# Kernel optimization log

Measured on AMD Instinct MI355X. Metric: run time of the kernel, lower is better.

Reference implementation:

```python
import jax, jax.numpy as jnp
import numpy as np


def setup_inputs() -> dict:
    key = jax.random.key(0)
    k1, k2, k3 = jax.random.split(key, 3)
    B, H, S, D = 4, 16, 2048, 64
    queries = jax.random.normal(k1, (B, H, S, D), dtype=jnp.float32)
    keys = jax.random.normal(k2, (B, H, S, D), dtype=jnp.float32)
    values = jax.random.normal(k3, (B, H, S, D), dtype=jnp.float32)
    return {"queries": queries, "keys": keys, "values": values, "d_k": D}


def reference(queries, keys, values, d_k):
    # scores = Q K^T / sqrt(d_k)  -> [B, H, S, S]
    scale = 1.0 / jnp.sqrt(jnp.asarray(d_k, dtype=queries.dtype))
    scores = jnp.einsum("bhqd,bhkd->bhqk", queries, keys) * scale
    weights = jax.nn.softmax(scores, axis=-1)
    # out = weights V -> [B, H, S, D]
    return jnp.einsum("bhqk,bhkd->bhqd", weights, values)
```

## Files before the change

kernel.cpp:

```cpp
#include <hip/hip_runtime.h>
#include <hip/hip_bf16.h>

typedef __attribute__((ext_vector_type(8))) short short8;
typedef __attribute__((ext_vector_type(4))) short short4v;
typedef __attribute__((ext_vector_type(16))) float f32x16;

constexpr int Sn = 2048, Dn = 64;
constexpr int KVB = 64;
constexpr int QB  = 256;
constexpr int NT  = Sn / KVB;
constexpr int KSTR = 72;
constexpr int VSTR = 68;
constexpr float QSC = 0.18033688011112042f;

struct SMemS { short K[2][KVB][KSTR]; short Vt[2][Dn][VSTR]; };
union  SMem  { SMemS s; float ep[4][32][36]; };

__device__ inline unsigned cvt_pk_bf16(float a, float b) {
  unsigned r;
  asm("v_cvt_pk_bf16_f32 %0, %1, %2" : "=v"(r) : "v"(a), "v"(b));
  return r;
}
__device__ inline short8 catw(unsigned a, unsigned b, unsigned c, unsigned d) {
  union { unsigned u[4]; short8 s; } t;
  t.u[0]=a; t.u[1]=b; t.u[2]=c; t.u[3]=d;
  return t.s;
}
__device__ inline short8 pack8(float4 a, float4 b) {
  return catw(cvt_pk_bf16(a.x,a.y), cvt_pk_bf16(a.z,a.w),
              cvt_pk_bf16(b.x,b.y), cvt_pk_bf16(b.z,b.w));
}
__device__ inline short8 cat4(short4v a, short4v b) {
  short8 r;
  r[0]=a[0]; r[1]=a[1]; r[2]=a[2]; r[3]=a[3];
  r[4]=b[0]; r[5]=b[1]; r[6]=b[2]; r[7]=b[3];
  return r;
}

__global__ __launch_bounds__(256, 2)
void attn_fwd(const float* __restrict__ Qm, const float* __restrict__ Km,
              const float* __restrict__ Vm, float* __restrict__ Om) {
  __shared__ alignas(16) SMem sm;

  const int fid = blockIdx.x + (blockIdx.y << 3);
  const int xcd = fid & 7, w = fid >> 3;
  const int qt = w & 7, bh = (xcd << 3) | (w >> 3);

  const size_t base = (size_t)bh * Sn * Dn;
  const float* Qb = Qm + base;
  const float* Kb = Km + base;
  const float* Vb = Vm + base;
  float*       Ob = Om + base;

  const int tid = threadIdx.x, wv = tid >> 6, lane = tid & 63;
  const int il = lane & 31, hi = lane >> 5;
  const int qr0 = qt * QB + wv * 64;

  short8 qf[2][4];
#pragma unroll
  for (int u = 0; u < 2; ++u)
#pragma unroll
    for (int ks = 0; ks < 4; ++ks) {
      const float4* qp = (const float4*)(Qb + (size_t)(qr0 + u*32 + il) * Dn + ks*16 + hi*8);
      float4 a = qp[0], b = qp[1];
      a.x*=QSC; a.y*=QSC; a.z*=QSC; a.w*=QSC;
      b.x*=QSC; b.y*=QSC; b.z*=QSC; b.w*=QSC;
      qf[u][ks] = pack8(a, b);
    }

  f32x16 acc[2][2];
#pragma unroll
  for (int u = 0; u < 2; ++u)
#pragma unroll
    for (int dt = 0; dt < 2; ++dt)
#pragma unroll
      for (int r = 0; r < 16; ++r) acc[u][dt][r] = 0.f;
  float m_run[2] = {-1e30f, -1e30f}, l_run[2] = {0.f, 0.f};

  f32x16 fz;
#pragma unroll
  for (int r = 0; r < 16; ++r) fz[r] = 0.f;

  const int krow = tid >> 2, kc = (tid & 3) * 16;
  const int vd = tid & 63, vk0 = (tid >> 6) * 8;

  auto stageK = [&](int buf, float4 a0, float4 a1, float4 a2, float4 a3) {
    *(short8*)&sm.s.K[buf][krow][kc]     = pack8(a0, a1);
    *(short8*)&sm.s.K[buf][krow][kc + 8] = pack8(a2, a3);
  };
  auto stageV = [&](int buf, const float* vv) {
#pragma unroll
    for (int c = 0; c < 2; ++c) {
      union { unsigned u[2]; short4v s; } t0, t1;
      t0.u[0] = cvt_pk_bf16(vv[c*8+0], vv[c*8+1]);
      t0.u[1] = cvt_pk_bf16(vv[c*8+2], vv[c*8+3]);
      t1.u[0] = cvt_pk_bf16(vv[c*8+4], vv[c*8+5]);
      t1.u[1] = cvt_pk_bf16(vv[c*8+6], vv[c*8+7]);
      short* p = &sm.s.Vt[buf][vd][vk0 + c*32];
      *(short4v*)p       = t0.s;
      *(short4v*)(p + 4) = t1.s;
    }
  };

  short8 pb[2][2][2];

  auto qk_sm = [&](int buf) {
    short8 kf[2][4];
#pragma unroll
    for (int h = 0; h < 2; ++h)
#pragma unroll
      for (int ks = 0; ks < 4; ++ks)
        kf[h][ks] = *(const short8*)&sm.s.K[buf][h*32 + il][ks*16 + hi*8];

    f32x16 sa[2][2];
#pragma unroll
    for (int u = 0; u < 2; ++u)
#pragma unroll
      for (int h = 0; h < 2; ++h) {
        sa[u][h] = __builtin_amdgcn_mfma_f32_32x32x16_bf16(kf[h][0], qf[u][0], fz, 0, 0, 0);
#pragma unroll
        for (int ks = 1; ks < 4; ++ks)
          sa[u][h] = __builtin_amdgcn_mfma_f32_32x32x16_bf16(kf[h][ks], qf[u][ks], sa[u][h], 0, 0, 0);
      }

#pragma unroll
    for (int u = 0; u < 2; ++u) {
      float tm[16];
#pragma unroll
      for (int r = 0; r < 16; ++r) tm[r] = fmaxf(sa[u][0][r], sa[u][1][r]);
#pragma unroll
      for (int s = 8; s > 0; s >>= 1)
#pragma unroll
        for (int r = 0; r < s; ++r) tm[r] = fmaxf(tm[r], tm[r + s]);
      float mx = fmaxf(tm[0], __shfl_xor(tm[0], 32));

      float mnew = fmaxf(m_run[u], mx);
      float corr = __builtin_amdgcn_exp2f(m_run[u] - mnew);
      m_run[u] = mnew;
      l_run[u] *= corr;
#pragma unroll
      for (int dt = 0; dt < 2; ++dt)
#pragma unroll
        for (int r = 0; r < 16; ++r) acc[u][dt][r] *= corr;

#pragma unroll
      for (int h = 0; h < 2; ++h)
#pragma unroll
        for (int r = 0; r < 16; ++r) sa[u][h][r] = __builtin_amdgcn_exp2f(sa[u][h][r] - mnew);
      float ta[16];
#pragma unroll
      for (int r = 0; r < 16; ++r) ta[r] = sa[u][0][r] + sa[u][1][r];
#pragma unroll
      for (int s = 8; s > 0; s >>= 1)
#pragma unroll
        for (int r = 0; r < s; ++r) ta[r] += ta[r + s];
      l_run[u] += ta[0] + __shfl_xor(ta[0], 32);

#pragma unroll
      for (int h = 0; h < 2; ++h) {
        pb[u][h][0] = catw(cvt_pk_bf16(sa[u][h][0],  sa[u][h][1]),  cvt_pk_bf16(sa[u][h][2],  sa[u][h][3]),
                           cvt_pk_bf16(sa[u][h][4],  sa[u][h][5]),  cvt_pk_bf16(sa[u][h][6],  sa[u][h][7]));
        pb[u][h][1] = catw(cvt_pk_bf16(sa[u][h][8],  sa[u][h][9]),  cvt_pk_bf16(sa[u][h][10], sa[u][h][11]),
                           cvt_pk_bf16(sa[u][h][12], sa[u][h][13]), cvt_pk_bf16(sa[u][h][14], sa[u][h][15]));
      }
    }
  };

  auto pv = [&](int buf) {
#pragma unroll
    for (int h = 0; h < 2; ++h)
#pragma unroll
      for (int dt = 0; dt < 2; ++dt) {
        const short* vrow = &sm.s.Vt[buf][dt*32 + il][h*32];
        short8 va = cat4(*(const short4v*)(vrow + 4*hi),      *(const short4v*)(vrow + 8  + 4*hi));
        short8 vb = cat4(*(const short4v*)(vrow + 16 + 4*hi), *(const short4v*)(vrow + 24 + 4*hi));
#pragma unroll
        for (int u = 0; u < 2; ++u) {
          acc[u][dt] = __builtin_amdgcn_mfma_f32_32x32x16_bf16(va, pb[u][h][0], acc[u][dt], 0, 0, 0);
          acc[u][dt] = __builtin_amdgcn_mfma_f32_32x32x16_bf16(vb, pb[u][h][1], acc[u][dt], 0, 0, 0);
        }
      }
  };

  {
    const float4* kp = (const float4*)(Kb + (size_t)krow * Dn + kc);
    float4 a0 = kp[0], a1 = kp[1], a2 = kp[2], a3 = kp[3];
    float vv[16];
#pragma unroll
    for (int c = 0; c < 2; ++c)
#pragma unroll
      for (int j = 0; j < 8; ++j) vv[c*8+j] = Vb[(size_t)(vk0 + c*32 + j) * Dn + vd];
    stageK(0, a0, a1, a2, a3);
    stageV(0, vv);
  }
  __syncthreads();

  int cur = 0;
#pragma unroll 1
  for (int t = 0; t < NT - 1; ++t) {
    const int kvn = (t + 1) * KVB;
    const float4* kp = (const float4*)(Kb + (size_t)(kvn + krow) * Dn + kc);
    float4 na0 = kp[0], na1 = kp[1], na2 = kp[2], na3 = kp[3];
    float nv[16];
#pragma unroll
    for (int c = 0; c < 2; ++c)
#pragma unroll
      for (int j = 0; j < 8; ++j) nv[c*8+j] = Vb[(size_t)(kvn + vk0 + c*32 + j) * Dn + vd];

    qk_sm(cur);
    stageK(cur ^ 1, na0, na1, na2, na3);
    stageV(cur ^ 1, nv);
    pv(cur);
    __syncthreads();
    cur ^= 1;
  }
  qk_sm(cur);
  pv(cur);
  __syncthreads();

  const int q2 = lane >> 1, dh = (lane & 1) * 16;
#pragma unroll
  for (int u = 0; u < 2; ++u) {
    const float inv = 1.0f / l_run[u];
#pragma unroll
    for (int dt = 0; dt < 2; ++dt) {
#pragma unroll
      for (int r = 0; r < 16; ++r) {
        int dcol = (r & 3) + 8 * (r >> 2) + 4 * hi;
        sm.ep[wv][il][dcol] = acc[u][dt][r] * inv;
      }
#pragma unroll
      for (int i = 0; i < 4; ++i) {
        float4 o = *(const float4*)&sm.ep[wv][q2][dh + i*4];
        *(float4*)(Ob + (size_t)(qr0 + u*32 + q2) * Dn + dt*32 + dh + i*4) = o;
      }
    }
  }
}

extern "C" void kernel_launch(void* const* d_in, const int* in_sizes, int n_in,
                              void* d_out, int out_size, void* d_ws, size_t ws_size,
                              hipStream_t stream) {
  const float* Q = (const float*)d_in[0];
  const float* K = (const float*)d_in[1];
  const float* V = (const float*)d_in[2];
  float* O = (float*)d_out;
  dim3 grid(Sn / QB, 4 * 16);
  attn_fwd<<<grid, 256, 0, stream>>>(Q, K, V, O);
}
```

Baseline: 104.4 us.

## Software-pipeline PV of previous tile with QK of current tile

```diff
diff --git a/kernel.cpp b/kernel.cpp
--- a/kernel.cpp
+++ b/kernel.cpp
@@ -76,6 +76,9 @@
 #pragma unroll
       for (int r = 0; r < 16; ++r) acc[u][dt][r] = 0.f;
   float m_run[2] = {-1e30f, -1e30f}, l_run[2] = {0.f, 0.f};
+  float corrp[2] = {0.f, 0.f};
+  short8 pb[2][2][2];
+  short8 vregs[8];
 
   f32x16 fz;
 #pragma unroll
@@ -84,35 +87,42 @@
   const int krow = tid >> 2, kc = (tid & 3) * 16;
   const int vd = tid & 63, vk0 = (tid >> 6) * 8;
 
-  auto stageK = [&](int buf, float4 a0, float4 a1, float4 a2, float4 a3) {
-    *(short8*)&sm.s.K[buf][krow][kc]     = pack8(a0, a1);
-    *(short8*)&sm.s.K[buf][krow][kc + 8] = pack8(a2, a3);
-  };
-  auto stageV = [&](int buf, const float* vv) {
+  auto loadK = [&](int t, short8& k0, short8& k1) {
+    const float4* kp = (const float4*)(Kb + (size_t)(t*KVB + krow) * Dn + kc);
+    k0 = pack8(kp[0], kp[1]);
+    k1 = pack8(kp[2], kp[3]);
+  };
+  auto loadV = [&](int t, short4v* v4) {
 #pragma unroll
     for (int c = 0; c < 2; ++c) {
+      float vv[8];
+#pragma unroll
+      for (int j = 0; j < 8; ++j) vv[j] = Vb[(size_t)(t*KVB + vk0 + c*32 + j) * Dn + vd];
       union { unsigned u[2]; short4v s; } t0, t1;
-      t0.u[0] = cvt_pk_bf16(vv[c*8+0], vv[c*8+1]);
-      t0.u[1] = cvt_pk_bf16(vv[c*8+2], vv[c*8+3]);
-      t1.u[0] = cvt_pk_bf16(vv[c*8+4], vv[c*8+5]);
-      t1.u[1] = cvt_pk_bf16(vv[c*8+6], vv[c*8+7]);
+      t0.u[0] = cvt_pk_bf16(vv[0], vv[1]); t0.u[1] = cvt_pk_bf16(vv[2], vv[3]);
+      t1.u[0] = cvt_pk_bf16(vv[4], vv[5]); t1.u[1] = cvt_pk_bf16(vv[6], vv[7]);
+      v4[c*2]   = t0.s;
+      v4[c*2+1] = t1.s;
+    }
+  };
+  auto writeKV = [&](int buf, short8 k0, short8 k1, const short4v* v4) {
+    *(short8*)&sm.s.K[buf][krow][kc]     = k0;
+    *(short8*)&sm.s.K[buf][krow][kc + 8] = k1;
+#pragma unroll
+    for (int c = 0; c < 2; ++c) {
       short* p = &sm.s.Vt[buf][vd][vk0 + c*32];
-      *(short4v*)p       = t0.s;
-      *(short4v*)(p + 4) = t1.s;
-    }
-  };
-
-  short8 pb[2][2][2];
-
-  auto qk_sm = [&](int buf) {
+      *(short4v*)p       = v4[c*2];
+      *(short4v*)(p + 4) = v4[c*2+1];
+    }
+  };
+
+  auto qk = [&](int buf, f32x16 sa[2][2]) {
     short8 kf[2][4];
 #pragma unroll
     for (int h = 0; h < 2; ++h)
 #pragma unroll
       for (int ks = 0; ks < 4; ++ks)
         kf[h][ks] = *(const short8*)&sm.s.K[buf][h*32 + il][ks*16 + hi*8];
-
-    f32x16 sa[2][2];
 #pragma unroll
     for (int u = 0; u < 2; ++u)
 #pragma unroll
@@ -122,7 +132,9 @@
         for (int ks = 1; ks < 4; ++ks)
           sa[u][h] = __builtin_amdgcn_mfma_f32_32x32x16_bf16(kf[h][ks], qf[u][ks], sa[u][h], 0, 0, 0);
       }
-
+  };
+
+  auto softmax = [&](f32x16 sa[2][2]) {
 #pragma unroll
     for (int u = 0; u < 2; ++u) {
       float tm[16];
@@ -137,12 +149,8 @@
       float mnew = fmaxf(m_run[u], mx);
       float corr = __builtin_amdgcn_exp2f(m_run[u] - mnew);
       m_run[u] = mnew;
+      corrp[u] = corr;
       l_run[u] *= corr;
-#pragma unroll
-      for (int dt = 0; dt < 2; ++dt)
-#pragma unroll
-        for (int r = 0; r < 16; ++r) acc[u][dt][r] *= corr;
-
 #pragma unroll
       for (int h = 0; h < 2; ++h)
 #pragma unroll
@@ -166,56 +174,77 @@
     }
   };
 
-  auto pv = [&](int buf) {
+  auto vload = [&](int buf) {
 #pragma unroll
     for (int h = 0; h < 2; ++h)
 #pragma unroll
       for (int dt = 0; dt < 2; ++dt) {
         const short* vrow = &sm.s.Vt[buf][dt*32 + il][h*32];
-        short8 va = cat4(*(const short4v*)(vrow + 4*hi),      *(const short4v*)(vrow + 8  + 4*hi));
-        short8 vb = cat4(*(const short4v*)(vrow + 16 + 4*hi), *(const short4v*)(vrow + 24 + 4*hi));
+        vregs[h*4 + dt*2 + 0] = cat4(*(const short4v*)(vrow + 4*hi),      *(const short4v*)(vrow + 8  + 4*hi));
+        vregs[h*4 + dt*2 + 1] = cat4(*(const short4v*)(vrow + 16 + 4*hi), *(const short4v*)(vrow + 24 + 4*hi));
+      }
+  };
+
+  auto pvr = [&]() {
+#pragma unroll
+    for (int u = 0; u < 2; ++u)
+#pragma unroll
+      for (int dt = 0; dt < 2; ++dt)
+#pragma unroll
+        for (int r = 0; r < 16; ++r) acc[u][dt][r] *= corrp[u];
+#pragma unroll
+    for (int h = 0; h < 2; ++h)
+#pragma unroll
+      for (int dt = 0; dt < 2; ++dt)
 #pragma unroll
         for (int u = 0; u < 2; ++u) {
-          acc[u][dt] = __builtin_amdgcn_mfma_f32_32x32x16_bf16(va, pb[u][h][0], acc[u][dt], 0, 0, 0);
-          acc[u][dt] = __builtin_amdgcn_mfma_f32_32x32x16_bf16(vb, pb[u][h][1], acc[u][dt], 0, 0, 0);
+          acc[u][dt] = __builtin_amdgcn_mfma_f32_32x32x16_bf16(vregs[h*4+dt*2+0], pb[u][h][0], acc[u][dt], 0, 0, 0);
+          acc[u][dt] = __builtin_amdgcn_mfma_f32_32x32x16_bf16(vregs[h*4+dt*2+1], pb[u][h][1], acc[u][dt], 0, 0, 0);
         }
-      }
   };
 
   {
-    const float4* kp = (const float4*)(Kb + (size_t)krow * Dn + kc);
-    float4 a0 = kp[0], a1 = kp[1], a2 = kp[2], a3 = kp[3];
-    float vv[16];
-#pragma unroll
-    for (int c = 0; c < 2; ++c)
-#pragma unroll
-      for (int j = 0; j < 8; ++j) vv[c*8+j] = Vb[(size_t)(vk0 + c*32 + j) * Dn + vd];
-    stageK(0, a0, a1, a2, a3);
-    stageV(0, vv);
+    short8 k0, k1; short4v v4[4];
+    loadK(0, k0, k1); loadV(0, v4);
+    writeKV(0, k0, k1, v4);
   }
   __syncthreads();
 
-  int cur = 0;
+  {
+    short8 k0, k1; short4v v4[4];
+    loadK(1, k0, k1); loadV(1, v4);
+    f32x16 sa[2][2];
+    qk(0, sa);
+    softmax(sa);
+    vload(0);
+    writeKV(1, k0, k1, v4);
+  }
+  __syncthreads();
+
 #pragma unroll 1
-  for (int t = 0; t < NT - 1; ++t) {
-    const int kvn = (t + 1) * KVB;
-    const float4* kp = (const float4*)(Kb + (size_t)(kvn + krow) * Dn + kc);
-    float4 na0 = kp[0], na1 = kp[1], na2 = kp[2], na3 = kp[3];
-    float nv[16];
-#pragma unroll
-    for (int c = 0; c < 2; ++c)
-#pragma unroll
-      for (int j = 0; j < 8; ++j) nv[c*8+j] = Vb[(size_t)(kvn + vk0 + c*32 + j) * Dn + vd];
-
-    qk_sm(cur);
-    stageK(cur ^ 1, na0, na1, na2, na3);
-    stageV(cur ^ 1, nv);
-    pv(cur);
+  for (int t = 1; t <= NT - 2; ++t) {
+    const int cur = t & 1;
+    short8 nk0, nk1; short4v nv4[4];
+    loadK(t + 1, nk0, nk1); loadV(t + 1, nv4);
+
+    pvr();
+    f32x16 sa[2][2];
+    qk(cur, sa);
+    softmax(sa);
+    vload(cur);
+    writeKV(cur ^ 1, nk0, nk1, nv4);
     __syncthreads();
-    cur ^= 1;
-  }
-  qk_sm(cur);
-  pv(cur);
+  }
+
+  {
+    const int cur = (NT - 1) & 1;
+    pvr();
+    f32x16 sa[2][2];
+    qk(cur, sa);
+    softmax(sa);
+    vload(cur);
+    pvr();
+  }
   __syncthreads();
 
   const int q2 = lane >> 1, dh = (lane & 1) * 16;
```

New measurement: 112.6 us. 7.9% more time.
